# Performance work log

Hardware: AMD Instinct MI355X
Metric: run time of the kernel (lower is better)

The kernel has to match this reference:

```python
import jax, jax.numpy as jnp
import numpy as np

K = 3          # kernel_size per pseudo-coordinate dim
DIM = 3        # edge_attr dimensionality
M = K ** DIM   # total number of spline kernel weight matrices


def spline_conv(x, src, dst, pseudo, W, Wr, b):
    """Degree-1 open B-spline conv (torch_geometric SplineConv, aggr='mean').
    x: (N, C_in), pseudo: (E, DIM) in [0,1], W: (M, C_in, C_out), Wr: (C_in, C_out), b: (C_out,).
    """
    N, C_in = x.shape
    pos = pseudo * (K - 1)                      # (E, DIM) in [0, K-1]
    i0 = jnp.clip(jnp.floor(pos), 0, K - 2)     # lower knot index per dim
    frac = pos - i0                             # (E, DIM) linear basis fraction
    i0 = i0.astype(jnp.int32)
    strides = jnp.array([1, K, K * K], dtype=jnp.int32)
    xj = x[src]                                 # (E, C_in) irregular gather
    # accumulate basis-weighted neighbor features per (dst node, kernel index)
    acc = jnp.zeros((N * M, C_in), dtype=x.dtype)
    for bits in range(2 ** DIM):                # 8 corners of the linear B-spline support
        off = jnp.array([(bits >> d) & 1 for d in range(DIM)], dtype=jnp.int32)
        w = jnp.prod(jnp.where(off == 1, frac, 1.0 - frac), axis=1)       # (E,)
        kidx = jnp.sum((i0 + off[None, :]) * strides[None, :], axis=1)    # (E,) flat kernel idx
        acc = acc.at[dst * M + kidx].add(w[:, None] * xj)                 # scatter-add
    out = jnp.einsum('nmi,mio->no', acc.reshape(N, M, C_in), W)
    deg = jnp.zeros((N,), x.dtype).at[dst].add(1.0)                        # in-degree
    out = out / jnp.maximum(deg, 1.0)[:, None]                             # mean aggregation
    return out + x @ Wr + b                                                # root weight + bias


def setup_inputs() -> dict:
    key = jax.random.key(0)
    ks = jax.random.split(key, 16)
    N, E = 50000, 800000
    dims = [3, 64, 64, 64]
    inp = {
        "x": jax.random.normal(ks[0], (N, 3), jnp.float32),
        "edge_index": jax.random.randint(ks[1], (2, E), 0, N),
        "edge_attr": jax.random.uniform(ks[2], (E, DIM), dtype=jnp.float32),
    }
    for l in range(3):
        ci, co = dims[l], dims[l + 1]
        inp[f"W{l}"] = jax.random.normal(ks[3 + 3 * l], (M, ci, co), jnp.float32) * (1.0 / np.sqrt(ci * M))
        inp[f"root{l}"] = jax.random.normal(ks[4 + 3 * l], (ci, co), jnp.float32) * (1.0 / np.sqrt(ci))
        inp[f"b{l}"] = jnp.zeros((co,), jnp.float32)
    return inp


def reference(x, edge_index, edge_attr, W0, root0, b0, W1, root1, b1, W2, root2, b2):
    src, dst = edge_index[0], edge_index[1]   # PyG flow: source_to_target
    h = x
    for W, Wr, b in ((W0, root0, b0), (W1, root1, b1), (W2, root2, b2)):
        h = jax.nn.relu(spline_conv(h, src, dst, edge_attr, W, Wr, b))
    return h
```

## Files before the change

kernel.cpp:

```cpp
#include <hip/hip_runtime.h>
#include <cstdint>


typedef __attribute__((ext_vector_type(8))) short short8;
typedef __attribute__((ext_vector_type(4))) float floatx4;

#define AS1 __attribute__((address_space(1)))
#define AS3 __attribute__((address_space(3)))

__device__ inline short f2bf(float f) {
    union { float f; unsigned u; } x; x.f = f;
    unsigned r = x.u + 0x7FFF + ((x.u >> 16) & 1);
    return (short)(r >> 16);
}

__device__ inline float bf2f(unsigned short u) {
    union { unsigned u; float f; } x;
    x.u = ((unsigned)u) << 16;
    return x.f;
}


__global__ void count_kernel(const int* __restrict__ ei, int* __restrict__ count, int E) {
    int e = blockIdx.x * blockDim.x + threadIdx.x;
    if (e < E) atomicAdd(&count[ei[E + e]], 1);
}

__global__ __launch_bounds__(1024) void scan_tile_kernel(const int* __restrict__ count,
                                                         int* __restrict__ row_ptr,
                                                         int* __restrict__ bsum, int N) {
    __shared__ int wsum[16];
    int tid = threadIdx.x, lane = tid & 63, wid = tid >> 6;
    int i = blockIdx.x * 1024 + tid;
    int v = (i < N) ? count[i] : 0;
    int incl = v;
#pragma unroll
    for (int off = 1; off < 64; off <<= 1) {
        int t = __shfl_up(incl, off, 64);
        if (lane >= off) incl += t;
    }
    if (lane == 63) wsum[wid] = incl;
    __syncthreads();
    if (tid < 16) {
        int w = wsum[tid];
#pragma unroll
        for (int off = 1; off < 16; off <<= 1) {
            int t = __shfl_up(w, off, 16);
            if ((tid & 15) >= off) w += t;
        }
        wsum[tid] = w;
    }
    __syncthreads();
    int waveoff = (wid > 0) ? wsum[wid - 1] : 0;
    if (i < N) row_ptr[i] = waveoff + incl - v;
    if (tid == 1023) bsum[blockIdx.x] = waveoff + incl;
}

__global__ __launch_bounds__(64) void scan_bsum_kernel(const int* __restrict__ bsum,
                                                       int* __restrict__ boff,
                                                       int* __restrict__ tot, int nb) {
    int tid = threadIdx.x;
    int v = (tid < nb) ? bsum[tid] : 0;
    int incl = v;
#pragma unroll
    for (int off = 1; off < 64; off <<= 1) {
        int t = __shfl_up(incl, off, 64);
        if (tid >= off) incl += t;
    }
    boff[tid] = incl - v;
    if (tid == 63) tot[0] = incl;
}

__global__ __launch_bounds__(1024) void scan_add_kernel(int* __restrict__ row_ptr,
                                                        const int* __restrict__ boff,
                                                        const int* __restrict__ tot,
                                                        int* __restrict__ cursor, int N) {
    int i = blockIdx.x * 1024 + threadIdx.x;
    if (i < N) {
        int r = row_ptr[i] + boff[blockIdx.x];
        row_ptr[i] = r;
        cursor[i] = r;
    }
    if (i == 0) row_ptr[N] = tot[0];
}

__global__ void basis_sort_kernel(const int* __restrict__ ei, const float* __restrict__ attr,
                                  const int* __restrict__ count, int* __restrict__ cursor,
                                  int* __restrict__ s_meta, float* __restrict__ s_w, int E) {
    int e = blockIdx.x * blockDim.x + threadIdx.x;
    if (e >= E) return;
    int src = ei[e];
    int dst = ei[E + e];
    float f[3]; int i0[3];
#pragma unroll
    for (int d = 0; d < 3; d++) {
        float pos = attr[e * 3 + d] * 2.0f;
        float fl = floorf(pos);
        fl = fminf(fmaxf(fl, 0.0f), 1.0f);
        i0[d] = (int)fl;
        f[d] = pos - fl;
    }
    int base = i0[0] + 3 * i0[1] + 9 * i0[2];
    float invd = 1.0f / fmaxf((float)count[dst], 1.0f);
    int p = atomicAdd(&cursor[dst], 1);
    s_meta[p] = src | (base << 24) | (i0[0] << 28) | (i0[1] << 29) | (i0[2] << 30);
    float w[8];
#pragma unroll
    for (int c = 0; c < 8; c++) {
        float ww = invd;
#pragma unroll
        for (int d = 0; d < 3; d++) {
            int off = (c >> d) & 1;
            ww *= off ? f[d] : (1.0f - f[d]);
        }
        w[c] = ww;
    }
    floatx4 w03 = {w[0], w[1], w[2], w[3]};
    floatx4 w47 = {w[4], w[5], w[6], w[7]};
    *(floatx4*)(s_w + (size_t)p * 8) = w03;
    *(floatx4*)(s_w + (size_t)p * 8 + 4) = w47;
}

__global__ void build_wb2(const float* __restrict__ Wa, const float* __restrict__ Ra,
                          unsigned short* __restrict__ wba,
                          const float* __restrict__ Wb, const float* __restrict__ Rb,
                          unsigned short* __restrict__ wbb) {
    int idx0 = blockIdx.x * blockDim.x + threadIdx.x;
    int half = idx0 / (4 * 56 * 64);
    if (half >= 2) return;
    int idx = idx0 - half * (4 * 56 * 64);
    const float* W = half ? Wb : Wa;
    const float* Wr = half ? Rb : Ra;
    unsigned short* wb = half ? wbb : wba;
    int l = idx & 63;
    int c = (idx >> 6) % 56;
    int t = idx / (56 * 64);
    int q = l >> 4, o = t * 16 + (l & 15);
    short8 out;
#pragma unroll
    for (int j = 0; j < 8; j++) {
        int k = c * 32 + q * 8 + j;
        float v = (k < 1728) ? W[(size_t)k * 64 + o] : Wr[(size_t)(k - 1728) * 64 + o];
        out[j] = f2bf(v);
    }
    *(short8*)(wb + (size_t)idx * 8) = out;
}

__global__ __launch_bounds__(256) void layer0_kernel(
    const float* __restrict__ x, const float* __restrict__ W0,
    const float* __restrict__ Wr, const float* __restrict__ bias,
    const int* __restrict__ row_ptr, const int* __restrict__ s_meta,
    const float* __restrict__ s_w, unsigned short* __restrict__ h_out, int N) {
    constexpr int NPB = 32, KT = 84;
    __shared__ __align__(16) float acc[NPB * 2 * KT];
    int tid = threadIdx.x, lane = tid & 63, wv = tid >> 6;
    int n0 = blockIdx.x * NPB;
    for (int k = tid; k < NPB * 2 * KT; k += 256) acc[k] = 0.0f;
    __syncthreads();

    int d = lane >> 5, hl = lane & 31;
    int c = hl / 3, i = hl - c * 3;
    bool act = (hl < 24);
    int cc = act ? c : 0;
    int coff = (c & 1) + 3 * ((c >> 1) & 1) + 9 * (c >> 2);

    for (int g2 = 0; g2 < 8; g2++) {
        int g = wv * 8 + g2;
        int n = n0 + g;
        if (n >= N) continue;
        if (lane < 3) acc[(g * 2) * KT + 81 + lane] = x[(size_t)n * 3 + lane];
        int rs = row_ptr[n], re = row_ptr[n + 1];
        int npairs = (re - rs + 1) >> 1;
        float* accd = &acc[(g * 2 + d) * KT];
        for (int pb = 0; pb < npairs; pb += 4) {
            int metas[4]; float ws_[4], xs_[4];
#pragma unroll
            for (int j = 0; j < 4; j++) {
                int ej = rs + (pb + j) * 2 + d;
                bool v = (pb + j < npairs) && (ej < re);
                int ec = v ? ej : rs;
                metas[j] = s_meta[ec];
                float wv_ = s_w[(size_t)ec * 8 + cc];
                ws_[j] = v ? wv_ : 0.0f;
            }
#pragma unroll
            for (int j = 0; j < 4; j++)
                xs_[j] = x[(size_t)(metas[j] & 0xFFFFFF) * 3 + i];
#pragma unroll
            for (int j = 0; j < 4; j++) {
                int kidx = ((metas[j] >> 24) & 0xF) + coff;
                if (act) accd[kidx * 3 + i] += ws_[j] * xs_[j];
            }
        }
    }
    __syncthreads();

    int o = lane;
    float wreg[KT];
#pragma unroll
    for (int k = 0; k < KT; k++)
        wreg[k] = (k < 81) ? W0[k * 64 + o] : Wr[(k - 81) * 64 + o];
    float bv = bias[o];
    for (int g = wv; g < NPB; g += 4) {
        int n = n0 + g;
        if (n >= N) break;
        float s = bv;
#pragma unroll
        for (int k4 = 0; k4 < KT; k4 += 4) {
            floatx4 a0 = *(const floatx4*)&acc[(g * 2) * KT + k4];
            floatx4 a1 = *(const floatx4*)&acc[(g * 2 + 1) * KT + k4];
            s += (a0.x + a1.x) * wreg[k4] + (a0.y + a1.y) * wreg[k4 + 1]
               + (a0.z + a1.z) * wreg[k4 + 2] + (a0.w + a1.w) * wreg[k4 + 3];
        }
        h_out[(size_t)n * 64 + o] = (unsigned short)f2bf(fmaxf(s, 0.0f));
    }
}

template <bool OUTF32>
__global__ __launch_bounds__(512, 4) void layer64_kernel(
    const unsigned short* __restrict__ h_in, const unsigned short* __restrict__ wb,
    const float* __restrict__ bias, const int* __restrict__ row_ptr,
    const int* __restrict__ s_meta, const float* __restrict__ s_w,
    void* __restrict__ h_out, int N) {
    constexpr int NPB = 8;
    constexpr int RGS = 3216;
    __shared__ __align__(16) unsigned short lds[NPB * RGS];
    int tid = threadIdx.x, lane = tid & 63;
    int wvu = __builtin_amdgcn_readfirstlane(tid >> 6);
    int n0 = blockIdx.x * NPB;
    int srow = lane & 15, sgrp = lane >> 4;

    unsigned short* reg = &lds[(size_t)wvu * RGS];
    unsigned short* featL = reg;
    float* w8fL = (float*)(reg + 2048);
    int* metaL = (int*)(reg + 3072);

    {
        int n = n0 + wvu;
        if (n >= N) {
            for (int k = lane; k < 1792; k += 64) reg[k] = 0;
        } else {
            int r0a = srow % 3, r1a = (srow / 3) % 3, r2a = srow / 9;
            int rb = srow + 16;
            int r0b = rb % 3, r1b = (rb / 3) % 3, r2b = rb / 9;
            bool rv1 = (srow < 11);

            floatx4 facc[2][4];
#pragma unroll
            for (int mt = 0; mt < 2; mt++)
#pragma unroll
                for (int nt = 0; nt < 4; nt++)
                    facc[mt][nt] = (floatx4){0.0f, 0.0f, 0.0f, 0.0f};

            int rs = row_ptr[n], re = row_ptr[n + 1];
            int deg = re - rs;
            for (int wbo = 0; wbo < deg; wbo += 64) {
                __builtin_amdgcn_global_load_lds(
                    (const AS1 unsigned int*)(s_meta + rs + wbo + lane),
                    (AS3 unsigned int*)metaL, 4, 0, 0);
#pragma unroll
                for (int k = 0; k < 2; k++) {
                    const float* wsrc = s_w + (size_t)(rs + wbo) * 8
                                      + k * 256 + lane * 4;
                    __builtin_amdgcn_global_load_lds(
                        (const AS1 unsigned int*)wsrc,
                        (AS3 unsigned int*)(w8fL + k * 256), 16, 0, 0);
                }
                asm volatile("s_waitcnt vmcnt(0)" ::: "memory");
                int dw = deg - wbo;
                int vmax = (dw < 64 ? dw : 64) - 1;
                for (int ch2 = 0; ch2 < 2; ch2++) {
                    int cb = ch2 * 32;
                    if (cb >= dw) break;
#pragma unroll
                    for (int i = 0; i < 4; i++) {
                        int el = cb + i * 8 + (lane >> 3);
                        if (el > vmax) el = vmax;
                        int ms = metaL[el] & 0xFFFFFF;
                        int c3 = (lane & 7) ^ i;
                        const unsigned short* srcp = h_in + (size_t)ms * 64 + c3 * 8;
                        __builtin_amdgcn_global_load_lds(
                            (const AS1 unsigned int*)srcp,
                            (AS3 unsigned int*)(featL + i * 512), 16, 0, 0);
                    }
                    short8 af0, af1;
#pragma unroll
                    for (int j = 0; j < 8; j++) {
                        int ec = cb + 8 * sgrp + j;
                        bool ve = ec < dw;
                        int m = metaL[ec];
                        int d0 = (m >> 28) & 1, d1 = (m >> 29) & 1, d2 = (m >> 30) & 1;
                        {
                            int c0 = r0a - d0, c1 = r1a - d1, c2 = r2a - d2;
                            bool vc = (((c0 | c1 | c2) & ~1) == 0) && ve;
                            int ci = (c0 + (c1 << 1) + (c2 << 2)) & 7;
                            float wf = w8fL[ec * 8 + ci];
                            af0[j] = vc ? f2bf(wf) : (short)0;
                        }
                        {
                            int c0 = r0b - d0, c1 = r1b - d1, c2 = r2b - d2;
                            bool vc = rv1 && (((c0 | c1 | c2) & ~1) == 0) && ve;
                            int ci = (c0 + (c1 << 1) + (c2 << 2)) & 7;
                            float wf = w8fL[ec * 8 + ci];
                            af1[j] = vc ? f2bf(wf) : (short)0;
                        }
                    }
                    asm volatile("s_waitcnt vmcnt(0)" ::: "memory");
#pragma unroll
                    for (int nt = 0; nt < 4; nt++) {
                        short8 bn;
#pragma unroll
                        for (int jj = 0; jj < 8; jj++) {
                            int e = sgrp * 8 + jj;
                            int g = e * 8 + (((nt * 2) + (srow >> 3)) ^ sgrp);
                            bn[jj] = (short)featL[g * 8 + (srow & 7)];
                        }
                        facc[0][nt] = __builtin_amdgcn_mfma_f32_16x16x32_bf16(
                            af0, bn, facc[0][nt], 0, 0, 0);
                        facc[1][nt] = __builtin_amdgcn_mfma_f32_16x16x32_bf16(
                            af1, bn, facc[1][nt], 0, 0, 0);
                    }
                }
            }
#pragma unroll
            for (int mt = 0; mt < 2; mt++)
#pragma unroll
                for (int nt = 0; nt < 4; nt++)
#pragma unroll
                    for (int r = 0; r < 4; r++) {
                        int mrow = mt * 16 + sgrp * 4 + r;
                        if (mrow < 27)
                            reg[mrow * 64 + nt * 16 + srow] =
                                (unsigned short)f2bf(facc[mt][nt][r]);
                    }
            reg[1728 + lane] = h_in[(size_t)n * 64 + lane];
        }
    }
    __syncthreads();

    {
        int t = wvu & 3;
        int hf = wvu >> 2;
        const unsigned short* ap = lds + (size_t)(lane & 7) * RGS + ((lane >> 4) * 8);
        floatx4 fpb = {0.0f, 0.0f, 0.0f, 0.0f};
        const unsigned short* wbp = wb + ((size_t)(t * 56) * 64 + lane) * 8;
#pragma unroll
        for (int ci = 0; ci < 28; ci++) {
            int c = hf * 28 + ci;
            short8 af = *(const short8*)(ap + c * 32);
            short8 bfr = *(const short8*)(wbp + (size_t)c * 64 * 8);
            fpb = __builtin_amdgcn_mfma_f32_16x16x32_bf16(af, bfr, fpb, 0, 0, 0);
        }
        __syncthreads();
        float* pfw = (float*)(lds + (size_t)wvu * RGS);
#pragma unroll
        for (int r = 0; r < 4; r++) pfw[r * 64 + lane] = fpb[r];
        __syncthreads();
        if (wvu < 4) {
            int o = t * 16 + (lane & 15);
            float bv = bias[o];
            const float* pft = (const float*)(lds + (size_t)t * RGS);
            const float* pfu = (const float*)(lds + (size_t)(t + 4) * RGS);
#pragma unroll
            for (int r = 0; r < 4; r++) {
                int m = (lane >> 4) * 4 + r;
                if (m < 8) {
                    int n = n0 + m;
                    if (n < N) {
                        float s = pft[r * 64 + lane] + pfu[r * 64 + lane];
                        float val = fmaxf(s + bv, 0.0f);
                        if (OUTF32) {
                            ((float*)h_out)[(size_t)n * 64 + o] = val;
                        } else {
                            ((unsigned short*)h_out)[(size_t)n * 64 + o] =
                                (unsigned short)f2bf(val);
                        }
                    }
                }
            }
        }
    }
}

extern "C" void kernel_launch(void* const* d_in, const int* in_sizes, int n_in,
                              void* d_out, int out_size, void* d_ws, size_t ws_size,
                              hipStream_t stream) {
    (void)n_in; (void)out_size; (void)ws_size;
    const float* x    = (const float*)d_in[0];
    const int*   ei   = (const int*)d_in[1];
    const float* attr = (const float*)d_in[2];
    const float* W0 = (const float*)d_in[3];
    const float* R0 = (const float*)d_in[4];
    const float* B0 = (const float*)d_in[5];
    const float* W1 = (const float*)d_in[6];
    const float* R1 = (const float*)d_in[7];
    const float* B1 = (const float*)d_in[8];
    const float* W2 = (const float*)d_in[9];
    const float* R2 = (const float*)d_in[10];
    const float* B2 = (const float*)d_in[11];
    const int N = in_sizes[0] / 3;
    const int E = in_sizes[1] / 2;

    char* ws = (char*)d_ws;
    size_t off = 0;
    auto alloc = [&](size_t bytes) {
        size_t cur = off;
        off = (off + bytes + 255) & ~(size_t)255;
        return cur;
    };
    int* row_ptr = (int*)(ws + alloc((size_t)(N + 1) * 4));
    int* count   = (int*)(ws + alloc((size_t)N * 4));
    int* cursor  = (int*)(ws + alloc((size_t)N * 4));
    int* bsum    = (int*)(ws + alloc(64 * 4));
    int* boff    = (int*)(ws + alloc(64 * 4));
    int* tot     = (int*)(ws + alloc(4));
    int* s_meta  = (int*)(ws + alloc((size_t)E * 4));
    float* s_w   = (float*)(ws + alloc((size_t)E * 8 * 4));
    unsigned short* h_a = (unsigned short*)(ws + alloc((size_t)N * 64 * 2));
    unsigned short* h_b = (unsigned short*)(ws + alloc((size_t)N * 64 * 2));
    unsigned short* wb1 = (unsigned short*)(ws + alloc((size_t)4 * 56 * 64 * 8 * 2));
    unsigned short* wb2 = (unsigned short*)(ws + alloc((size_t)4 * 56 * 64 * 8 * 2));

    int nb = (N + 1023) / 1024;

    hipMemsetAsync(count, 0, (size_t)N * 4, stream);
    count_kernel<<<(E + 255) / 256, 256, 0, stream>>>(ei, count, E);
    scan_tile_kernel<<<nb, 1024, 0, stream>>>(count, row_ptr, bsum, N);
    scan_bsum_kernel<<<1, 64, 0, stream>>>(bsum, boff, tot, nb);
    scan_add_kernel<<<nb, 1024, 0, stream>>>(row_ptr, boff, tot, cursor, N);
    basis_sort_kernel<<<(E + 255) / 256, 256, 0, stream>>>(ei, attr, count, cursor,
                                                           s_meta, s_w, E);
    build_wb2<<<(2 * 4 * 56 * 64 + 255) / 256, 256, 0, stream>>>(W1, R1, wb1,
                                                                 W2, R2, wb2);

    layer0_kernel<<<(N + 31) / 32, 256, 0, stream>>>(x, W0, R0, B0, row_ptr,
                                                     s_meta, s_w, h_a, N);
    layer64_kernel<false><<<(N + 7) / 8, 512, 0, stream>>>(h_a, wb1, B1, row_ptr,
                                                           s_meta, s_w, h_b, N);
    layer64_kernel<true><<<(N + 7) / 8, 512, 0, stream>>>(h_b, wb2, B2, row_ptr,
                                                          s_meta, s_w, d_out, N);
}
```

Baseline: 441.1 us.

## Overlap meta/weight loads with feature gathers, change LDS swizzle, halve final GEMM waves

The full vmcnt(0) wait after the meta and weight loads becomes a partial wait, so only the meta index loads must finish before the feature gathers are issued. The weight loads are then waited on after the gathers are in flight. The LDS swizzle for the gathered features changes from XOR with i to XOR with i<<1, which alters the bank conflict pattern on the B-fragment reads. The final dense GEMM stage now runs on 4 waves that each compute two output tiles sharing one A fragment, instead of 8 waves with one tile each. This reduces A-fragment LDS reads but leaves half the waves idle in that stage.

```diff
diff --git a/kernel.cpp b/kernel.cpp
--- a/kernel.cpp
+++ b/kernel.cpp
@@ -266,9 +266,10 @@
                         (const AS1 unsigned int*)wsrc,
                         (AS3 unsigned int*)(w8fL + k * 256), 16, 0, 0);
                 }
-                asm volatile("s_waitcnt vmcnt(0)" ::: "memory");
+                asm volatile("s_waitcnt vmcnt(2)" ::: "memory");
                 int dw = deg - wbo;
                 int vmax = (dw < 64 ? dw : 64) - 1;
+                bool firstchunk = true;
                 for (int ch2 = 0; ch2 < 2; ch2++) {
                     int cb = ch2 * 32;
                     if (cb >= dw) break;
@@ -277,11 +278,15 @@
                         int el = cb + i * 8 + (lane >> 3);
                         if (el > vmax) el = vmax;
                         int ms = metaL[el] & 0xFFFFFF;
-                        int c3 = (lane & 7) ^ i;
+                        int c3 = (lane & 7) ^ (i << 1);
                         const unsigned short* srcp = h_in + (size_t)ms * 64 + c3 * 8;
                         __builtin_amdgcn_global_load_lds(
                             (const AS1 unsigned int*)srcp,
                             (AS3 unsigned int*)(featL + i * 512), 16, 0, 0);
+                    }
+                    if (firstchunk) {
+                        asm volatile("s_waitcnt vmcnt(4)" ::: "memory");
+                        firstchunk = false;
                     }
                     short8 af0, af1;
 #pragma unroll
@@ -312,7 +317,7 @@
 #pragma unroll
                         for (int jj = 0; jj < 8; jj++) {
                             int e = sgrp * 8 + jj;
-                            int g = e * 8 + (((nt * 2) + (srow >> 3)) ^ sgrp);
+                            int g = e * 8 + (((nt * 2) + (srow >> 3)) ^ (sgrp << 1));
                             bn[jj] = (short)featL[g * 8 + (srow & 7)];
                         }
                         facc[0][nt] = __builtin_amdgcn_mfma_f32_16x16x32_bf16(
@@ -339,35 +344,49 @@
     __syncthreads();
 
     {
-        int t = wvu & 3;
-        int hf = wvu >> 2;
-        const unsigned short* ap = lds + (size_t)(lane & 7) * RGS + ((lane >> 4) * 8);
-        floatx4 fpb = {0.0f, 0.0f, 0.0f, 0.0f};
-        const unsigned short* wbp = wb + ((size_t)(t * 56) * 64 + lane) * 8;
-#pragma unroll
-        for (int ci = 0; ci < 28; ci++) {
-            int c = hf * 28 + ci;
-            short8 af = *(const short8*)(ap + c * 32);
-            short8 bfr = *(const short8*)(wbp + (size_t)c * 64 * 8);
-            fpb = __builtin_amdgcn_mfma_f32_16x16x32_bf16(af, bfr, fpb, 0, 0, 0);
-        }
-        __syncthreads();
-        float* pfw = (float*)(lds + (size_t)wvu * RGS);
-#pragma unroll
-        for (int r = 0; r < 4; r++) pfw[r * 64 + lane] = fpb[r];
+        floatx4 f0 = {0.0f, 0.0f, 0.0f, 0.0f};
+        floatx4 f1 = {0.0f, 0.0f, 0.0f, 0.0f};
+        if (wvu < 4) {
+            int hf = wvu >> 1;
+            int tp = wvu & 1;
+            const unsigned short* ap = lds + (size_t)(lane & 7) * RGS + ((lane >> 4) * 8);
+            const unsigned short* wbp0 = wb + ((size_t)((tp * 2) * 56) * 64 + lane) * 8;
+            const unsigned short* wbp1 = wb + ((size_t)((tp * 2 + 1) * 56) * 64 + lane) * 8;
+#pragma unroll
+            for (int ci = 0; ci < 28; ci++) {
+                int c = hf * 28 + ci;
+                short8 af = *(const short8*)(ap + c * 32);
+                short8 b0 = *(const short8*)(wbp0 + (size_t)c * 64 * 8);
+                short8 b1 = *(const short8*)(wbp1 + (size_t)c * 64 * 8);
+                f0 = __builtin_amdgcn_mfma_f32_16x16x32_bf16(af, b0, f0, 0, 0, 0);
+                f1 = __builtin_amdgcn_mfma_f32_16x16x32_bf16(af, b1, f1, 0, 0, 0);
+            }
+        }
         __syncthreads();
         if (wvu < 4) {
+            float* pfw = (float*)(lds + (size_t)wvu * RGS);
+#pragma unroll
+            for (int r = 0; r < 4; r++) {
+                pfw[r * 64 + lane] = f0[r];
+                pfw[256 + r * 64 + lane] = f1[r];
+            }
+        }
+        __syncthreads();
+        if (wvu < 4) {
+            int t = wvu;
             int o = t * 16 + (lane & 15);
             float bv = bias[o];
-            const float* pft = (const float*)(lds + (size_t)t * RGS);
-            const float* pfu = (const float*)(lds + (size_t)(t + 4) * RGS);
+            const float* pfA = (const float*)(lds + (size_t)(t >> 1) * RGS)
+                             + (t & 1) * 256;
+            const float* pfB = (const float*)(lds + (size_t)(2 + (t >> 1)) * RGS)
+                             + (t & 1) * 256;
 #pragma unroll
             for (int r = 0; r < 4; r++) {
                 int m = (lane >> 4) * 4 + r;
                 if (m < 8) {
                     int n = n0 + m;
                     if (n < N) {
-                        float s = pft[r * 64 + lane] + pfu[r * 64 + lane];
+                        float s = pfA[r * 64 + lane] + pfB[r * 64 + lane];
                         float val = fmaxf(s + bv, 0.0f);
                         if (OUTF32) {
                             ((float*)h_out)[(size_t)n * 64 + o] = val;
```

Result: no change. 435.2 us (-1.3%).
